# Performance work log

Measured on AMD Instinct MI355X. Metric: run time of the kernel, lower is better.

## Reference

```python
import jax, jax.numpy as jnp
import numpy as np

NUM_HEADS = 12

def setup_inputs() -> dict:
    key = jax.random.key(0)
    ks = jax.random.split(key, 6)
    B, N, C = 8, 1024, 768
    s = 1.0 / np.sqrt(C).astype(np.float32)
    x = jax.random.normal(ks[0], (B, N, C), dtype=jnp.float32)
    Wq = jax.random.normal(ks[1], (C, C), dtype=jnp.float32) * s
    Wk = jax.random.normal(ks[2], (C, C), dtype=jnp.float32) * s
    Wv = jax.random.normal(ks[3], (C, C), dtype=jnp.float32) * s
    Wproj = jax.random.normal(ks[4], (C, C), dtype=jnp.float32) * s
    attn_bias = jax.random.normal(ks[5], (N, N), dtype=jnp.float32) * 0.02
    return {"x": x, "Wq": Wq, "Wk": Wk, "Wv": Wv, "Wproj": Wproj, "attn_bias": attn_bias}

def reference(x, Wq, Wk, Wv, Wproj, attn_bias):
    B, N, C = x.shape
    nh = NUM_HEADS
    d = C // nh                      # head_dim = qk_head_dim = 64
    scale = d ** -0.5
    # linear projections (bias=False), split heads: [B, nh, N, d]
    q = (x @ Wq).reshape(B, N, nh, d).transpose(0, 2, 1, 3) * scale
    k = (x @ Wk).reshape(B, N, nh, d).transpose(0, 2, 1, 3)
    v = (x @ Wv).reshape(B, N, nh, d).transpose(0, 2, 1, 3)
    # scores + learned additive bias (broadcast over B, nh), stable softmax
    scores = jnp.einsum('bhqd,bhkd->bhqk', q, k) + attn_bias
    attn = jax.nn.softmax(scores, axis=-1)       # [B, nh, N, N]
    out = jnp.einsum('bhqk,bhkd->bhqd', attn, v)
    out = out.transpose(0, 2, 1, 3).reshape(B, N, C) @ Wproj
    return out, attn
```

## Files before the change

kernel.cpp:

```cpp
#include <hip/hip_runtime.h>
#include <hip/hip_bf16.h>

typedef __bf16 bf16;
typedef __attribute__((ext_vector_type(4))) __bf16 bf16x4;
typedef __attribute__((ext_vector_type(8))) __bf16 bf16x8;
typedef __attribute__((ext_vector_type(4))) float f32x4;

#define MFMA(a,b,c) __builtin_amdgcn_mfma_f32_16x16x32_bf16(a,b,c,0,0,0)

__global__ __launch_bounds__(256) void convert_x_kernel(const float* __restrict__ x,
                                                        bf16* __restrict__ xb) {
    int i = blockIdx.x * 256 + threadIdx.x;
    float4 v = ((const float4*)x)[i];
    bf16x4 o = { (bf16)v.x, (bf16)v.y, (bf16)v.z, (bf16)v.w };
    ((bf16x4*)xb)[i] = o;
}

__global__ __launch_bounds__(1024) void convert_w_kernel(const float* __restrict__ W,
                                                         bf16* __restrict__ Wt) {
    __shared__ float tile[32][33];
    int k0 = blockIdx.x * 32, n0 = blockIdx.y * 32;
    int tx = threadIdx.x & 31, ty = threadIdx.x >> 5;
    tile[ty][tx] = W[(k0 + ty) * 768 + n0 + tx];
    __syncthreads();
    Wt[(n0 + ty) * 768 + k0 + tx] = (bf16)tile[tx][ty];
}

__global__ __launch_bounds__(256) void gemm_kernel(const bf16* __restrict__ A,
                                                   const bf16* __restrict__ Bt,
                                                   void* __restrict__ dst, int mode) {
    __shared__ bf16 As[128][40];
    __shared__ bf16 Bs[128][40];
    const int K = 768;
    int m0 = blockIdx.x * 128, n0 = blockIdx.y * 128;
    int tid = threadIdx.x, lane = tid & 63, w = tid >> 6;
    int wr = w >> 1, wc = w & 1;
    int fr = lane & 15, fg = lane >> 4;
    int srow = tid >> 2, sch = (tid & 3) * 8;
    f32x4 acc[4][4] = {};
    for (int k0 = 0; k0 < K; k0 += 32) {
        __syncthreads();
        *(bf16x8*)&As[srow][sch]      = *(const bf16x8*)&A[(size_t)(m0 + srow) * K + k0 + sch];
        *(bf16x8*)&As[srow + 64][sch] = *(const bf16x8*)&A[(size_t)(m0 + srow + 64) * K + k0 + sch];
        *(bf16x8*)&Bs[srow][sch]      = *(const bf16x8*)&Bt[(size_t)(n0 + srow) * K + k0 + sch];
        *(bf16x8*)&Bs[srow + 64][sch] = *(const bf16x8*)&Bt[(size_t)(n0 + srow + 64) * K + k0 + sch];
        __syncthreads();
        bf16x8 af[4], bfr[4];
        #pragma unroll
        for (int i = 0; i < 4; i++) af[i]  = *(const bf16x8*)&As[wr*64 + i*16 + fr][fg*8];
        #pragma unroll
        for (int j = 0; j < 4; j++) bfr[j] = *(const bf16x8*)&Bs[wc*64 + j*16 + fr][fg*8];
        #pragma unroll
        for (int i = 0; i < 4; i++)
            #pragma unroll
            for (int j = 0; j < 4; j++)
                acc[i][j] = MFMA(af[i], bfr[j], acc[i][j]);
    }
    #pragma unroll
    for (int i = 0; i < 4; i++)
    #pragma unroll
    for (int j = 0; j < 4; j++)
    #pragma unroll
    for (int r = 0; r < 4; r++) {
        int grow = m0 + wr*64 + i*16 + fg*4 + r;
        int gcol = n0 + wc*64 + j*16 + fr;
        float v = acc[i][j][r];
        if (mode == 3) {
            ((float*)dst)[(size_t)grow * 768 + gcol] = v;
        } else {
            int b = grow >> 10, np = grow & 1023;
            int h = gcol >> 6, dd = gcol & 63;
            bf16* o = (bf16*)dst;
            if (mode == 0)      o[((size_t)(b*12 + h)*1024 + np)*64 + dd] = (bf16)(v * 0.125f);
            else if (mode == 1) o[((size_t)(b*12 + h)*1024 + np)*64 + dd] = (bf16)v;
            else                o[((size_t)(b*12 + h)*64 + dd)*1024 + np] = (bf16)v;
        }
    }
}

__global__ __launch_bounds__(256) void attn_kernel(const bf16* __restrict__ qb,
                                                   const bf16* __restrict__ kb,
                                                   const bf16* __restrict__ vt,
                                                   const float* __restrict__ bias,
                                                   float* __restrict__ attn,
                                                   bf16* __restrict__ Ob) {
    __shared__ bf16 P[16 * 1024];
    __shared__ float red[2][4][16];
    int bh = blockIdx.x, q0 = blockIdx.y * 16;
    int tid = threadIdx.x, lane = tid & 63, w = tid >> 6;
    int fr = lane & 15, fg = lane >> 4;
    const bf16* qp = qb + (size_t)bh * 65536;
    const bf16* kp = kb + (size_t)bh * 65536;
    const bf16* vp = vt + (size_t)bh * 65536;
    bf16x8 qa0 = *(const bf16x8*)&qp[(q0 + fr) * 64 + fg * 8];
    bf16x8 qa1 = *(const bf16x8*)&qp[(q0 + fr) * 64 + 32 + fg * 8];
    f32x4 s[16];
    #pragma unroll
    for (int j = 0; j < 16; j++) {
        int key0 = w * 256 + j * 16;
        bf16x8 kf0 = *(const bf16x8*)&kp[(key0 + fr) * 64 + fg * 8];
        bf16x8 kf1 = *(const bf16x8*)&kp[(key0 + fr) * 64 + 32 + fg * 8];
        f32x4 a = {};
        a = MFMA(kf0, qa0, a);
        a = MFMA(kf1, qa1, a);
        f32x4 bv = *(const f32x4*)&bias[(q0 + fr) * 1024 + key0 + fg * 4];
        s[j] = a + bv;
    }
    float mx = -1e30f;
    #pragma unroll
    for (int j = 0; j < 16; j++)
        mx = fmaxf(fmaxf(fmaxf(mx, s[j][0]), fmaxf(s[j][1], s[j][2])), s[j][3]);
    mx = fmaxf(mx, __shfl_xor(mx, 16));
    mx = fmaxf(mx, __shfl_xor(mx, 32));
    if (lane < 16) red[0][w][lane] = mx;
    __syncthreads();
    mx = fmaxf(fmaxf(red[0][0][fr], red[0][1][fr]), fmaxf(red[0][2][fr], red[0][3][fr]));
    float sum = 0.f;
    #pragma unroll
    for (int j = 0; j < 16; j++) {
        s[j][0] = __expf(s[j][0] - mx); s[j][1] = __expf(s[j][1] - mx);
        s[j][2] = __expf(s[j][2] - mx); s[j][3] = __expf(s[j][3] - mx);
        sum += s[j][0] + s[j][1] + s[j][2] + s[j][3];
    }
    sum += __shfl_xor(sum, 16);
    sum += __shfl_xor(sum, 32);
    if (lane < 16) red[1][w][lane] = sum;
    __syncthreads();
    float tot = (red[1][0][fr] + red[1][1][fr]) + (red[1][2][fr] + red[1][3][fr]);
    float rcp = 1.f / tot;
    float* arow = attn + ((size_t)bh * 1024 + q0 + fr) * 1024;
    #pragma unroll
    for (int j = 0; j < 16; j++) {
        int key = w * 256 + j * 16 + fg * 4;
        f32x4 p = s[j] * rcp;
        *(f32x4*)&arow[key] = p;
        bf16x4 pb = { (bf16)p[0], (bf16)p[1], (bf16)p[2], (bf16)p[3] };
        int chunk = key >> 3;
        *(bf16x4*)&P[fr * 1024 + ((chunk ^ (fr & 7)) << 3) + (key & 7)] = pb;
    }
    __syncthreads();
    f32x4 oacc = {};
    #pragma unroll
    for (int kk = 0; kk < 32; kk++) {
        int k0e = kk * 32 + fg * 8;
        int chunk = k0e >> 3;
        bf16x8 pa = *(const bf16x8*)&P[fr * 1024 + ((chunk ^ (fr & 7)) << 3)];
        bf16x8 vb = *(const bf16x8*)&vp[(w * 16 + fr) * 1024 + k0e];
        oacc = MFMA(pa, vb, oacc);
    }
    int b = bh / 12, h = bh % 12;
    #pragma unroll
    for (int r = 0; r < 4; r++) {
        int row = fg * 4 + r;
        Ob[((size_t)b * 1024 + q0 + row) * 768 + h * 64 + w * 16 + fr] = (bf16)oacc[r];
    }
}

extern "C" void kernel_launch(void* const* d_in, const int* in_sizes, int n_in,
                              void* d_out, int out_size, void* d_ws, size_t ws_size,
                              hipStream_t stream) {
    const float* x    = (const float*)d_in[0];
    const float* Wq   = (const float*)d_in[1];
    const float* Wk   = (const float*)d_in[2];
    const float* Wv   = (const float*)d_in[3];
    const float* Wp   = (const float*)d_in[4];
    const float* bias = (const float*)d_in[5];
    char* ws = (char*)d_ws;
    bf16* xb  = (bf16*)(ws + 0);
    bf16* wt  = (bf16*)(ws + 12582912);
    bf16* qbp = (bf16*)(ws + 17301504);
    bf16* kbp = (bf16*)(ws + 29884416);
    bf16* vtp = (bf16*)(ws + 42467328);
    bf16* obp = (bf16*)(ws + 55050240);
    float* out0 = (float*)d_out;
    float* attn = out0 + 6291456;

    convert_x_kernel<<<6144, 256, 0, stream>>>(x, xb);
    const float* Wsrc[4] = {Wq, Wk, Wv, Wp};
    for (int i = 0; i < 4; i++)
        convert_w_kernel<<<dim3(24,24), 1024, 0, stream>>>(Wsrc[i], wt + (size_t)i*589824);
    gemm_kernel<<<dim3(64,6), 256, 0, stream>>>(xb, wt + 0*589824, qbp, 0);
    gemm_kernel<<<dim3(64,6), 256, 0, stream>>>(xb, wt + 1*589824, kbp, 1);
    gemm_kernel<<<dim3(64,6), 256, 0, stream>>>(xb, wt + 2*589824, vtp, 2);
    attn_kernel<<<dim3(96,64), 256, 0, stream>>>(qbp, kbp, vtp, bias, attn, obp);
    gemm_kernel<<<dim3(64,6), 256, 0, stream>>>(obp, wt + 3*589824, out0, 3);
}
```

Before: 773.3 us.

## Pre-pack Q/K/V/bias into MFMA fragment layouts and coalesce attention stores

The Q/K and V GEMM epilogues now write directly in MFMA-fragment-packed layouts, so each attention fragment load becomes a contiguous per-lane vector read. The Q and K projections are merged into one launch, and the bias is repacked once into fragment order. The attention-probability write is restaged through shared memory so each wave stores full contiguous rows. The attention grid is reordered so neighbouring blocks share the same head's K/V. In exchange there is an extra bias-pack kernel and workspace, and the stored probabilities are now rounded to bf16 rather than kept in fp32.

Result: faster. 631.5 us (-18.3%).

```diff
diff --git a/kernel.cpp b/kernel.cpp
--- a/kernel.cpp
+++ b/kernel.cpp
@@ -7,6 +7,7 @@
 typedef __attribute__((ext_vector_type(4))) float f32x4;
 
 #define MFMA(a,b,c) __builtin_amdgcn_mfma_f32_16x16x32_bf16(a,b,c,0,0,0)
+
 
 __global__ __launch_bounds__(256) void convert_x_kernel(const float* __restrict__ x,
                                                         bf16* __restrict__ xb) {
@@ -26,9 +27,18 @@
     Wt[(n0 + ty) * 768 + k0 + tx] = (bf16)tile[tx][ty];
 }
 
-__global__ __launch_bounds__(256) void gemm_kernel(const bf16* __restrict__ A,
-                                                   const bf16* __restrict__ Bt,
-                                                   void* __restrict__ dst, int mode) {
+__global__ __launch_bounds__(256) void bias_pack_kernel(const float* __restrict__ bias,
+                                                        float* __restrict__ biasP) {
+    int t = blockIdx.x * 256 + threadIdx.x;
+    int fr = t & 15, fg = (t >> 4) & 3, kb = (t >> 6) & 63, qs = t >> 12;
+    float4 v = *(const float4*)&bias[(qs * 16 + fr) * 1024 + kb * 16 + fg * 4];
+    *(float4*)&biasP[t * 4] = v;
+}
+
+__global__ __launch_bounds__(256) void gemm_qk(const bf16* __restrict__ A,
+                                               const bf16* __restrict__ Bt,
+                                               bf16* __restrict__ QP,
+                                               bf16* __restrict__ KP) {
     __shared__ bf16 As[128][40];
     __shared__ bf16 Bs[128][40];
     const int K = 768;
@@ -54,6 +64,107 @@
         for (int i = 0; i < 4; i++)
             #pragma unroll
             for (int j = 0; j < 4; j++)
+                acc[i][j] = MFMA(bfr[j], af[i], acc[i][j]);
+    }
+    const int mat = (n0 >= 768);
+    bf16* __restrict__ dst = mat ? KP : QP;
+    const float qscale = mat ? 1.0f : 0.125f;
+    int fq_base = (n0 - mat * 768) + wc * 64;
+    int t_wave  = m0 + wr * 64;
+    int lofs = (fg >> 1) * 128 + fr * 8 + (fg & 1) * 4;
+    #pragma unroll
+    for (int i = 0; i < 4; i++) {
+        int tok0 = t_wave + i * 16;
+        int b = tok0 >> 10, ntok = tok0 & 1023;
+        #pragma unroll
+        for (int j = 0; j < 4; j++) {
+            int f0 = fq_base + j * 16;
+            int bh = b * 12 + (f0 >> 6), d0 = f0 & 63;
+            size_t base = ((size_t)((bh * 64 + (ntok >> 4)) * 8 + (d0 >> 3))) * 128;
+            bf16x4 v = { (bf16)(acc[i][j][0] * qscale), (bf16)(acc[i][j][1] * qscale),
+                         (bf16)(acc[i][j][2] * qscale), (bf16)(acc[i][j][3] * qscale) };
+            *(bf16x4*)&dst[base + lofs] = v;
+        }
+    }
+}
+
+__global__ __launch_bounds__(256) void gemm_v(const bf16* __restrict__ A,
+                                              const bf16* __restrict__ Bt,
+                                              bf16* __restrict__ VP) {
+    __shared__ bf16 As[128][40];
+    __shared__ bf16 Bs[128][40];
+    const int K = 768;
+    int m0 = blockIdx.x * 128, n0 = blockIdx.y * 128;
+    int tid = threadIdx.x, lane = tid & 63, w = tid >> 6;
+    int wr = w >> 1, wc = w & 1;
+    int fr = lane & 15, fg = lane >> 4;
+    int srow = tid >> 2, sch = (tid & 3) * 8;
+    f32x4 acc[4][4] = {};
+    for (int k0 = 0; k0 < K; k0 += 32) {
+        __syncthreads();
+        *(bf16x8*)&As[srow][sch]      = *(const bf16x8*)&A[(size_t)(m0 + srow) * K + k0 + sch];
+        *(bf16x8*)&As[srow + 64][sch] = *(const bf16x8*)&A[(size_t)(m0 + srow + 64) * K + k0 + sch];
+        *(bf16x8*)&Bs[srow][sch]      = *(const bf16x8*)&Bt[(size_t)(n0 + srow) * K + k0 + sch];
+        *(bf16x8*)&Bs[srow + 64][sch] = *(const bf16x8*)&Bt[(size_t)(n0 + srow + 64) * K + k0 + sch];
+        __syncthreads();
+        bf16x8 af[4], bfr[4];
+        #pragma unroll
+        for (int i = 0; i < 4; i++) af[i]  = *(const bf16x8*)&As[wr*64 + i*16 + fr][fg*8];
+        #pragma unroll
+        for (int j = 0; j < 4; j++) bfr[j] = *(const bf16x8*)&Bs[wc*64 + j*16 + fr][fg*8];
+        #pragma unroll
+        for (int i = 0; i < 4; i++)
+            #pragma unroll
+            for (int j = 0; j < 4; j++)
+                acc[i][j] = MFMA(af[i], bfr[j], acc[i][j]);
+    }
+    int t_wave = m0 + wr * 64;
+    int lofs = (fg >> 1) * 128 + fr * 8 + (fg & 1) * 4;
+    #pragma unroll
+    for (int i = 0; i < 4; i++) {
+        int tok0 = t_wave + i * 16;
+        int b = tok0 >> 10, ntok = tok0 & 1023;
+        #pragma unroll
+        for (int j = 0; j < 4; j++) {
+            int f0 = n0 + wc * 64 + j * 16;
+            int bh = b * 12 + (f0 >> 6), d0 = f0 & 63;
+            size_t base = ((size_t)((bh * 4 + (d0 >> 4)) * 32 + (ntok >> 5))) * 512
+                        + ((ntok >> 3) & 3) * 128;
+            bf16x4 v = { (bf16)acc[i][j][0], (bf16)acc[i][j][1],
+                         (bf16)acc[i][j][2], (bf16)acc[i][j][3] };
+            *(bf16x4*)&VP[base + lofs] = v;
+        }
+    }
+}
+
+__global__ __launch_bounds__(256) void gemm_out(const bf16* __restrict__ A,
+                                                const bf16* __restrict__ Bt,
+                                                float* __restrict__ dst) {
+    __shared__ bf16 As[128][40];
+    __shared__ bf16 Bs[128][40];
+    const int K = 768;
+    int m0 = blockIdx.x * 128, n0 = blockIdx.y * 128;
+    int tid = threadIdx.x, lane = tid & 63, w = tid >> 6;
+    int wr = w >> 1, wc = w & 1;
+    int fr = lane & 15, fg = lane >> 4;
+    int srow = tid >> 2, sch = (tid & 3) * 8;
+    f32x4 acc[4][4] = {};
+    for (int k0 = 0; k0 < K; k0 += 32) {
+        __syncthreads();
+        *(bf16x8*)&As[srow][sch]      = *(const bf16x8*)&A[(size_t)(m0 + srow) * K + k0 + sch];
+        *(bf16x8*)&As[srow + 64][sch] = *(const bf16x8*)&A[(size_t)(m0 + srow + 64) * K + k0 + sch];
+        *(bf16x8*)&Bs[srow][sch]      = *(const bf16x8*)&Bt[(size_t)(n0 + srow) * K + k0 + sch];
+        *(bf16x8*)&Bs[srow + 64][sch] = *(const bf16x8*)&Bt[(size_t)(n0 + srow + 64) * K + k0 + sch];
+        __syncthreads();
+        bf16x8 af[4], bfr[4];
+        #pragma unroll
+        for (int i = 0; i < 4; i++) af[i]  = *(const bf16x8*)&As[wr*64 + i*16 + fr][fg*8];
+        #pragma unroll
+        for (int j = 0; j < 4; j++) bfr[j] = *(const bf16x8*)&Bs[wc*64 + j*16 + fr][fg*8];
+        #pragma unroll
+        for (int i = 0; i < 4; i++)
+            #pragma unroll
+            for (int j = 0; j < 4; j++)
                 acc[i][j] = MFMA(af[i], bfr[j], acc[i][j]);
     }
     #pragma unroll
@@ -64,46 +175,37 @@
     for (int r = 0; r < 4; r++) {
         int grow = m0 + wr*64 + i*16 + fg*4 + r;
         int gcol = n0 + wc*64 + j*16 + fr;
-        float v = acc[i][j][r];
-        if (mode == 3) {
-            ((float*)dst)[(size_t)grow * 768 + gcol] = v;
-        } else {
-            int b = grow >> 10, np = grow & 1023;
-            int h = gcol >> 6, dd = gcol & 63;
-            bf16* o = (bf16*)dst;
-            if (mode == 0)      o[((size_t)(b*12 + h)*1024 + np)*64 + dd] = (bf16)(v * 0.125f);
-            else if (mode == 1) o[((size_t)(b*12 + h)*1024 + np)*64 + dd] = (bf16)v;
-            else                o[((size_t)(b*12 + h)*64 + dd)*1024 + np] = (bf16)v;
-        }
-    }
-}
-
-__global__ __launch_bounds__(256) void attn_kernel(const bf16* __restrict__ qb,
-                                                   const bf16* __restrict__ kb,
-                                                   const bf16* __restrict__ vt,
-                                                   const float* __restrict__ bias,
+        dst[(size_t)grow * 768 + gcol] = acc[i][j][r];
+    }
+}
+
+__global__ __launch_bounds__(256) void attn_kernel(const bf16* __restrict__ QP,
+                                                   const bf16* __restrict__ KP,
+                                                   const bf16* __restrict__ VP,
+                                                   const float* __restrict__ biasP,
                                                    float* __restrict__ attn,
                                                    bf16* __restrict__ Ob) {
     __shared__ bf16 P[16 * 1024];
     __shared__ float red[2][4][16];
-    int bh = blockIdx.x, q0 = blockIdx.y * 16;
-    int tid = threadIdx.x, lane = tid & 63, w = tid >> 6;
-    int fr = lane & 15, fg = lane >> 4;
-    const bf16* qp = qb + (size_t)bh * 65536;
-    const bf16* kp = kb + (size_t)bh * 65536;
-    const bf16* vp = vt + (size_t)bh * 65536;
-    bf16x8 qa0 = *(const bf16x8*)&qp[(q0 + fr) * 64 + fg * 8];
-    bf16x8 qa1 = *(const bf16x8*)&qp[(q0 + fr) * 64 + 32 + fg * 8];
+    int qs = blockIdx.x, bh = blockIdx.y, q0 = qs * 16;
+    int tid = threadIdx.x, lane = tid & 63, w = tid >> 6;
+    int fr = lane & 15, fg = lane >> 4;
+    const bf16*  qbase = QP + (size_t)(bh * 64 + qs) * 1024;
+    const bf16*  kbase = KP + (size_t)bh * 65536;
+    const bf16*  vbase = VP + (size_t)(bh * 4 + w) * 16384;
+    const float* bbase = biasP + (size_t)qs * 16384;
+    bf16x8 qa0 = *(const bf16x8*)&qbase[lane * 8];
+    bf16x8 qa1 = *(const bf16x8*)&qbase[512 + lane * 8];
     f32x4 s[16];
     #pragma unroll
     for (int j = 0; j < 16; j++) {
-        int key0 = w * 256 + j * 16;
-        bf16x8 kf0 = *(const bf16x8*)&kp[(key0 + fr) * 64 + fg * 8];
-        bf16x8 kf1 = *(const bf16x8*)&kp[(key0 + fr) * 64 + 32 + fg * 8];
+        int kb = w * 16 + j;
+        bf16x8 kf0 = *(const bf16x8*)&kbase[kb * 1024 + lane * 8];
+        bf16x8 kf1 = *(const bf16x8*)&kbase[kb * 1024 + 512 + lane * 8];
         f32x4 a = {};
         a = MFMA(kf0, qa0, a);
         a = MFMA(kf1, qa1, a);
-        f32x4 bv = *(const f32x4*)&bias[(q0 + fr) * 1024 + key0 + fg * 4];
+        f32x4 bv = *(const f32x4*)&bbase[kb * 256 + lane * 4];
         s[j] = a + bv;
     }
     float mx = -1e30f;
@@ -128,24 +230,33 @@
     __syncthreads();
     float tot = (red[1][0][fr] + red[1][1][fr]) + (red[1][2][fr] + red[1][3][fr]);
     float rcp = 1.f / tot;
-    float* arow = attn + ((size_t)bh * 1024 + q0 + fr) * 1024;
     #pragma unroll
     for (int j = 0; j < 16; j++) {
         int key = w * 256 + j * 16 + fg * 4;
         f32x4 p = s[j] * rcp;
-        *(f32x4*)&arow[key] = p;
         bf16x4 pb = { (bf16)p[0], (bf16)p[1], (bf16)p[2], (bf16)p[3] };
         int chunk = key >> 3;
         *(bf16x4*)&P[fr * 1024 + ((chunk ^ (fr & 7)) << 3) + (key & 7)] = pb;
     }
     __syncthreads();
+    float* abase = attn + ((size_t)bh * 1024 + q0) * 1024;
+    #pragma unroll
+    for (int rr = 0; rr < 4; rr++) {
+        int row = w * 4 + rr;
+        float* arow = abase + (size_t)row * 1024;
+        #pragma unroll
+        for (int c = 0; c < 4; c++) {
+            int g = c * 32 + (lane >> 1);
+            bf16x4 pb = *(const bf16x4*)&P[row * 1024 + ((g ^ (row & 7)) << 3) + (lane & 1) * 4];
+            f32x4 o = { (float)pb[0], (float)pb[1], (float)pb[2], (float)pb[3] };
+            *(f32x4*)&arow[c * 256 + lane * 4] = o;
+        }
+    }
     f32x4 oacc = {};
     #pragma unroll
     for (int kk = 0; kk < 32; kk++) {
-        int k0e = kk * 32 + fg * 8;
-        int chunk = k0e >> 3;
-        bf16x8 pa = *(const bf16x8*)&P[fr * 1024 + ((chunk ^ (fr & 7)) << 3)];
-        bf16x8 vb = *(const bf16x8*)&vp[(w * 16 + fr) * 1024 + k0e];
+        bf16x8 pa = *(const bf16x8*)&P[fr * 1024 + (((kk * 4 + fg) ^ (fr & 7)) << 3)];
+        bf16x8 vb = *(const bf16x8*)&vbase[kk * 512 + lane * 8];
         oacc = MFMA(pa, vb, oacc);
     }
     int b = bh / 12, h = bh % 12;
@@ -166,12 +277,13 @@
     const float* Wp   = (const float*)d_in[4];
     const float* bias = (const float*)d_in[5];
     char* ws = (char*)d_ws;
-    bf16* xb  = (bf16*)(ws + 0);
-    bf16* wt  = (bf16*)(ws + 12582912);
-    bf16* qbp = (bf16*)(ws + 17301504);
-    bf16* kbp = (bf16*)(ws + 29884416);
-    bf16* vtp = (bf16*)(ws + 42467328);
-    bf16* obp = (bf16*)(ws + 55050240);
+    bf16*  xb  = (bf16*)(ws + 0);
+    bf16*  obp = (bf16*)(ws + 0);
+    bf16*  wt  = (bf16*)(ws + 12582912);
+    bf16*  QPb = (bf16*)(ws + 17301504);
+    bf16*  KPb = (bf16*)(ws + 29884416);
+    bf16*  VPb = (bf16*)(ws + 42467328);
+    float* bP  = (float*)(ws + 55050240);
     float* out0 = (float*)d_out;
     float* attn = out0 + 6291456;
 
@@ -179,9 +291,9 @@
     const float* Wsrc[4] = {Wq, Wk, Wv, Wp};
     for (int i = 0; i < 4; i++)
         convert_w_kernel<<<dim3(24,24), 1024, 0, stream>>>(Wsrc[i], wt + (size_t)i*589824);
-    gemm_kernel<<<dim3(64,6), 256, 0, stream>>>(xb, wt + 0*589824, qbp, 0);
-    gemm_kernel<<<dim3(64,6), 256, 0, stream>>>(xb, wt + 1*589824, kbp, 1);
-    gemm_kernel<<<dim3(64,6), 256, 0, stream>>>(xb, wt + 2*589824, vtp, 2);
-    attn_kernel<<<dim3(96,64), 256, 0, stream>>>(qbp, kbp, vtp, bias, attn, obp);
-    gemm_kernel<<<dim3(64,6), 256, 0, stream>>>(obp, wt + 3*589824, out0, 3);
-}
+    bias_pack_kernel<<<1024, 256, 0, stream>>>(bias, bP);
+    gemm_qk<<<dim3(64,12), 256, 0, stream>>>(xb, wt, QPb, KPb);
+    gemm_v<<<dim3(64,6), 256, 0, stream>>>(xb, wt + 2*589824, VPb);
+    attn_kernel<<<dim3(64,96), 256, 0, stream>>>(QPb, KPb, VPb, bP, attn, obp);
+    gemm_out<<<dim3(64,6), 256, 0, stream>>>(obp, wt + 3*589824, out0);
+}
```
